# Kernel optimization log

Hardware: AMD Instinct MI355X
Metric: run time of the kernel (lower is better)

Reference implementation:

```python
import jax, jax.numpy as jnp
import numpy as np

H = 128  # hidden_size

def setup_inputs() -> dict:
    key = jax.random.key(0)
    ks = jax.random.split(key, 12)
    B, SEQ = 256, 1000
    static = jax.random.normal(ks[0], (B, 2, SEQ), jnp.float32)
    dynamic = jax.random.uniform(ks[1], (B, 2, SEQ), jnp.float32)
    # Encoder = 1x1 Conv1d(in_ch -> H): weight (H, in_ch), bias (H,)
    def xavier(k, shape):
        fan_in, fan_out = shape[1], shape[0]
        lim = np.sqrt(6.0 / (fan_in + fan_out)).astype(np.float32)
        return jax.random.uniform(k, shape, jnp.float32, -lim, lim)
    enc_s_w = xavier(ks[2], (H, 2)); enc_s_b = jnp.zeros((H,), jnp.float32)
    enc_d_w = xavier(ks[3], (H, 2)); enc_d_b = jnp.zeros((H,), jnp.float32)
    v = xavier(ks[4], (1, H))[0]                 # attention vector (H,)
    W = xavier(ks[5], (H, 3 * H))                # attention matrix (H, 3H)
    dense_w = xavier(ks[6], (H, 128)); dense_b = jnp.zeros((H,), jnp.float32)
    lin_w = xavier(ks[7], (1, H)); lin_b = jnp.zeros((1,), jnp.float32)
    return {"static": static, "dynamic": dynamic,
            "enc_s_w": enc_s_w, "enc_s_b": enc_s_b,
            "enc_d_w": enc_d_w, "enc_d_b": enc_d_b,
            "v": v, "W": W,
            "dense_w": dense_w, "dense_b": dense_b,
            "lin_w": lin_w, "lin_b": lin_b}


def reference(static, dynamic, enc_s_w, enc_s_b, enc_d_w, enc_d_b,
              v, W, dense_w, dense_b, lin_w, lin_b):
    B = static.shape[0]
    # 1x1-conv encoders (computed once; identical across loop iterations)
    e = jnp.einsum('hc,bcs->bhs', enc_s_w, static) + enc_s_b[None, :, None]   # (B,H,S)
    dyn_ld = jnp.broadcast_to(dynamic[:, 1:2, :], dynamic.shape)              # load channel expanded
    d = jnp.einsum('hc,bcs->bhs', enc_d_w, dyn_ld) + enc_d_b[None, :, None]   # (B,H,S)
    hy = jnp.zeros((B, H), static.dtype)
    for _ in range(3):  # fixed 3-step refinement loop
        hidden = jnp.concatenate(
            [e, d, jnp.broadcast_to(hy[:, :, None], e.shape)], axis=1)        # (B,3H,S)
        u = jnp.tanh(jnp.einsum('hk,bks->bhs', W, hidden))                    # (B,H,S)
        logit = jnp.einsum('h,bhs->bs', v, u)                                 # (B,S)
        prob = jax.nn.softmax(logit, axis=-1)
        hy = jnp.einsum('bs,bhs->bh', prob, e)                                # context update
    out = jax.nn.relu(hy @ dense_w.T + dense_b) @ lin_w.T + lin_b             # (B,1)
    return out
```

## Files before the change

kernel.cpp:

```cpp
#include <hip/hip_runtime.h>
#include <math.h>

#define HH  128
#define SS  1000
#define NT  1024
#define NW  (NT / 64)
#define C1 2.8853900817779268f
#define C2 1.4426950408889634f

typedef float v2f __attribute__((ext_vector_type(2)));

template <int CTRL>
__device__ __forceinline__ float dpp_add(float x) {
    int s = __builtin_amdgcn_update_dpp(0, __builtin_bit_cast(int, x),
                                        CTRL, 0xF, 0xF, true);
    return x + __builtin_bit_cast(float, s);
}


__global__ __launch_bounds__(NT) void sc_fold(
    const float* __restrict__ enc_s_w, const float* __restrict__ enc_s_b,
    const float* __restrict__ enc_d_w, const float* __restrict__ enc_d_b,
    const float* __restrict__ v, const float* __restrict__ W,
    float* __restrict__ ws) {
    const int t  = threadIdx.x;
    const int fh = blockIdx.x * 32 + (t >> 5);
    const int fq = t & 31;
    const float4* W1 = (const float4*)(W + fh * (3 * HH));
    const float4* W2 = (const float4*)(W + fh * (3 * HH) + HH);
    const float4* W3 = (const float4*)(W + fh * (3 * HH) + 2 * HH);
    const float4* ES = (const float4*)enc_s_w;
    const float4* ED = (const float4*)enc_d_w;
    const float4* SB = (const float4*)enc_s_b;
    const float4* DB = (const float4*)enc_d_b;
    const int k4 = fq;
    float4 w1 = W1[k4], w2 = W2[k4], w3 = W3[k4];
    float4 e01 = ES[2 * k4], e23 = ES[2 * k4 + 1];
    float4 d01 = ED[2 * k4], d23 = ED[2 * k4 + 1];
    float4 sb = SB[k4], db = DB[k4];
    float a0 = 0.f, a1 = 0.f, ad = 0.f, cc = 0.f, w30 = 0.f, w31 = 0.f, w3b = 0.f;
    a0 = fmaf(w1.x, e01.x, a0); a0 = fmaf(w1.y, e01.z, a0);
    a0 = fmaf(w1.z, e23.x, a0); a0 = fmaf(w1.w, e23.z, a0);
    a1 = fmaf(w1.x, e01.y, a1); a1 = fmaf(w1.y, e01.w, a1);
    a1 = fmaf(w1.z, e23.y, a1); a1 = fmaf(w1.w, e23.w, a1);
    ad = fmaf(w2.x, d01.x + d01.y, ad); ad = fmaf(w2.y, d01.z + d01.w, ad);
    ad = fmaf(w2.z, d23.x + d23.y, ad); ad = fmaf(w2.w, d23.z + d23.w, ad);
    cc = fmaf(w1.x, sb.x, cc); cc = fmaf(w1.y, sb.y, cc);
    cc = fmaf(w1.z, sb.z, cc); cc = fmaf(w1.w, sb.w, cc);
    cc = fmaf(w2.x, db.x, cc); cc = fmaf(w2.y, db.y, cc);
    cc = fmaf(w2.z, db.z, cc); cc = fmaf(w2.w, db.w, cc);
    w30 = fmaf(w3.x, e01.x, w30); w30 = fmaf(w3.y, e01.z, w30);
    w30 = fmaf(w3.z, e23.x, w30); w30 = fmaf(w3.w, e23.z, w30);
    w31 = fmaf(w3.x, e01.y, w31); w31 = fmaf(w3.y, e01.w, w31);
    w31 = fmaf(w3.z, e23.y, w31); w31 = fmaf(w3.w, e23.w, w31);
    w3b = fmaf(w3.x, sb.x, w3b); w3b = fmaf(w3.y, sb.y, w3b);
    w3b = fmaf(w3.z, sb.z, w3b); w3b = fmaf(w3.w, sb.w, w3b);
    a0  = dpp_add<0x111>(a0);  a0  = dpp_add<0x112>(a0);  a0  = dpp_add<0x114>(a0);
    a0  = dpp_add<0x118>(a0);  a0  = dpp_add<0x142>(a0);
    a1  = dpp_add<0x111>(a1);  a1  = dpp_add<0x112>(a1);  a1  = dpp_add<0x114>(a1);
    a1  = dpp_add<0x118>(a1);  a1  = dpp_add<0x142>(a1);
    ad  = dpp_add<0x111>(ad);  ad  = dpp_add<0x112>(ad);  ad  = dpp_add<0x114>(ad);
    ad  = dpp_add<0x118>(ad);  ad  = dpp_add<0x142>(ad);
    cc  = dpp_add<0x111>(cc);  cc  = dpp_add<0x112>(cc);  cc  = dpp_add<0x114>(cc);
    cc  = dpp_add<0x118>(cc);  cc  = dpp_add<0x142>(cc);
    w30 = dpp_add<0x111>(w30); w30 = dpp_add<0x112>(w30); w30 = dpp_add<0x114>(w30);
    w30 = dpp_add<0x118>(w30); w30 = dpp_add<0x142>(w30);
    w31 = dpp_add<0x111>(w31); w31 = dpp_add<0x112>(w31); w31 = dpp_add<0x114>(w31);
    w31 = dpp_add<0x118>(w31); w31 = dpp_add<0x142>(w31);
    w3b = dpp_add<0x111>(w3b); w3b = dpp_add<0x112>(w3b); w3b = dpp_add<0x114>(w3b);
    w3b = dpp_add<0x118>(w3b); w3b = dpp_add<0x142>(w3b);
    if (fq == 31) {
        ws[0 * HH + fh] = a0 * C1;
        ws[1 * HH + fh] = a1 * C1;
        ws[2 * HH + fh] = ad * C1;
        ws[4 * HH + fh] = cc * C1;
        ws[5 * HH + fh] = (cc + w3b) * C1;
        ws[6 * HH + fh] = w30 * C1;
        ws[7 * HH + fh] = w31 * C1;
    }
    if (blockIdx.x == 0) {
        if (t < HH) ws[3 * HH + t] = v[t];
        if (t < 32) {
            float4 x = ((const float4*)v)[t];
            float s = (x.x + x.y) + (x.z + x.w);
            #pragma unroll
            for (int off = 1; off < 32; off <<= 1) s += __shfl_xor(s, off);
            if (t == 0) ws[8 * HH] = s * C2;
        }
    }
}

#define OCTET(X, ACC)                                                         \
    {                                                                         \
        v2f vx0 = {X.x, X.x}, vx1 = {X.y, X.y}, vyv = {X.z, X.z};             \
        v2f z0 = __builtin_elementwise_fma(a0_0, vx0,                         \
                 __builtin_elementwise_fma(a1_0, vx1,                         \
                 __builtin_elementwise_fma(ad_0, vyv, cg_0)));                \
        v2f z1 = __builtin_elementwise_fma(a0_1, vx0,                         \
                 __builtin_elementwise_fma(a1_1, vx1,                         \
                 __builtin_elementwise_fma(ad_1, vyv, cg_1)));                \
        v2f z2 = __builtin_elementwise_fma(a0_2, vx0,                         \
                 __builtin_elementwise_fma(a1_2, vx1,                         \
                 __builtin_elementwise_fma(ad_2, vyv, cg_2)));                \
        v2f z3 = __builtin_elementwise_fma(a0_3, vx0,                         \
                 __builtin_elementwise_fma(a1_3, vx1,                         \
                 __builtin_elementwise_fma(ad_3, vyv, cg_3)));                \
        z0 = __builtin_elementwise_min(z0, clampv);                           \
        z1 = __builtin_elementwise_min(z1, clampv);                           \
        z2 = __builtin_elementwise_min(z2, clampv);                           \
        z3 = __builtin_elementwise_min(z3, clampv);                           \
        float e0 = __builtin_amdgcn_exp2f(z0.x);                              \
        float e1 = __builtin_amdgcn_exp2f(z0.y);                              \
        float e2 = __builtin_amdgcn_exp2f(z1.x);                              \
        float e3 = __builtin_amdgcn_exp2f(z1.y);                              \
        float e4 = __builtin_amdgcn_exp2f(z2.x);                              \
        float e5 = __builtin_amdgcn_exp2f(z2.y);                              \
        float e6 = __builtin_amdgcn_exp2f(z3.x);                              \
        float e7 = __builtin_amdgcn_exp2f(z3.y);                              \
        float tb0 = 1.f + e1, tb1 = 1.f + e3, tb2 = 1.f + e5, tb3 = 1.f + e7; \
        float d0 = fmaf(e0, tb0, tb0);                                        \
        float d1 = fmaf(e2, tb1, tb1);                                        \
        float d2 = fmaf(e4, tb2, tb2);                                        \
        float d3 = fmaf(e6, tb3, tb3);                                        \
        float n0 = fmaf(vv_0.x, e1, fmaf(vv_0.y, e0, cp0));                   \
        float n1 = fmaf(vv_1.x, e3, fmaf(vv_1.y, e2, cp1));                   \
        float n2 = fmaf(vv_2.x, e5, fmaf(vv_2.y, e4, cp2));                   \
        float n3 = fmaf(vv_3.x, e7, fmaf(vv_3.y, e6, cp3));                   \
        float Nq0 = fmaf(n0, d1, n1 * d0), Dq0 = d0 * d1;                     \
        float Nq1 = fmaf(n2, d3, n3 * d2), Dq1 = d2 * d3;                     \
        float Noc = fmaf(Nq0, Dq1, Nq1 * Dq0);                                \
        ACC = Noc * __builtin_amdgcn_rcpf(Dq0 * Dq1);                         \
        ACC = dpp_add<0x111>(ACC);                                            \
        ACC = dpp_add<0x112>(ACC);                                            \
        ACC = dpp_add<0x114>(ACC);                                            \
        ACC = dpp_add<0x118>(ACC);                                            \
    }

__global__ __launch_bounds__(NT, 4) void sc_main(
    const float* __restrict__ stat, const float* __restrict__ dyn,
    const float* __restrict__ ws,
    const float* __restrict__ enc_s_w, const float* __restrict__ enc_s_b,
    const float* __restrict__ dense_w, const float* __restrict__ dense_b,
    const float* __restrict__ lin_w, const float* __restrict__ lin_b,
    float* __restrict__ out) {
    const int b    = blockIdx.x;
    const int t    = threadIdx.x;
    const int wave = t >> 6;
    const int lane = t & 63;
    const int gl   = t & 15;
    const int sg   = t >> 4;

    __shared__ __align__(16) float4 xs[NT];
    __shared__ float4 red4[2][NW];
    __shared__ float hy_sh[HH];

    {
        float x0 = 0.f, x1 = 0.f, yv = 0.f;
        if (t < SS) {
            const float* sbp = stat + (size_t)b * 2 * SS;
            x0 = sbp[t];
            x1 = sbp[SS + t];
            yv = dyn[(size_t)b * 2 * SS + SS + t];
        }
        xs[t] = make_float4(x0, x1, yv, 0.f);
    }

    const int h0 = gl * 8;
    float4 u, u2;
    u = *(const float4*)(ws + 0 * HH + h0); u2 = *(const float4*)(ws + 0 * HH + h0 + 4);
    const v2f a0_0 = {u.x, u.y},  a0_1 = {u.z, u.w},
              a0_2 = {u2.x, u2.y}, a0_3 = {u2.z, u2.w};
    u = *(const float4*)(ws + 1 * HH + h0); u2 = *(const float4*)(ws + 1 * HH + h0 + 4);
    const v2f a1_0 = {u.x, u.y},  a1_1 = {u.z, u.w},
              a1_2 = {u2.x, u2.y}, a1_3 = {u2.z, u2.w};
    u = *(const float4*)(ws + 2 * HH + h0); u2 = *(const float4*)(ws + 2 * HH + h0 + 4);
    const v2f ad_0 = {u.x, u.y},  ad_1 = {u.z, u.w},
              ad_2 = {u2.x, u2.y}, ad_3 = {u2.z, u2.w};
    u = *(const float4*)(ws + 3 * HH + h0); u2 = *(const float4*)(ws + 3 * HH + h0 + 4);
    const v2f vv_0 = {u.x, u.y},  vv_1 = {u.z, u.w},
              vv_2 = {u2.x, u2.y}, vv_3 = {u2.z, u2.w};
    const float cp0 = vv_0.x + vv_0.y, cp1 = vv_1.x + vv_1.y;
    const float cp2 = vv_2.x + vv_2.y, cp3 = vv_3.x + vv_3.y;
    const float svc2 = ws[8 * HH];
    const v2f clampv = {14.f, 14.f};
    const bool ownerBase = (gl == 15);

    __syncthreads();

    float X0 = 0.f, X1 = 0.f;

    for (int iter = 0; iter < 3; ++iter) {
        v2f cg_0, cg_1, cg_2, cg_3;
        if (iter == 0) {
            u = *(const float4*)(ws + 4 * HH + h0);
            u2 = *(const float4*)(ws + 4 * HH + h0 + 4);
            cg_0 = (v2f){u.x, u.y};  cg_1 = (v2f){u.z, u.w};
            cg_2 = (v2f){u2.x, u2.y}; cg_3 = (v2f){u2.z, u2.w};
        } else {
            float4 b1 = *(const float4*)(ws + 5 * HH + h0);
            float4 b2 = *(const float4*)(ws + 5 * HH + h0 + 4);
            float4 p1 = *(const float4*)(ws + 6 * HH + h0);
            float4 p2 = *(const float4*)(ws + 6 * HH + h0 + 4);
            float4 q1 = *(const float4*)(ws + 7 * HH + h0);
            float4 q2 = *(const float4*)(ws + 7 * HH + h0 + 4);
            v2f X0v = {X0, X0}, X1v = {X1, X1};
            cg_0 = __builtin_elementwise_fma(
                (v2f){p1.x, p1.y}, X0v,
                __builtin_elementwise_fma((v2f){q1.x, q1.y}, X1v, (v2f){b1.x, b1.y}));
            cg_1 = __builtin_elementwise_fma(
                (v2f){p1.z, p1.w}, X0v,
                __builtin_elementwise_fma((v2f){q1.z, q1.w}, X1v, (v2f){b1.z, b1.w}));
            cg_2 = __builtin_elementwise_fma(
                (v2f){p2.x, p2.y}, X0v,
                __builtin_elementwise_fma((v2f){q2.x, q2.y}, X1v, (v2f){b2.x, b2.y}));
            cg_3 = __builtin_elementwise_fma(
                (v2f){p2.z, p2.w}, X0v,
                __builtin_elementwise_fma((v2f){q2.z, q2.w}, X1v, (v2f){b2.z, b2.w}));
        }

        float S = 0.f, Sx0 = 0.f, Sx1 = 0.f;
        #pragma unroll 2
        for (int pass = 0; pass < 8; ++pass) {
            const int sA = pass * 64 + sg;
            const int sB = 512 + sA;
            float4 xA = xs[sA];
            float4 xB = xs[sB];
            float accA, accB;
            OCTET(xA, accA);
            OCTET(xB, accB);
            float argA = ownerBase ? fmaf(-C1, accA, svc2) : -200.f;
            const bool ownB = ownerBase && (sB < SS);
            float argB = ownB ? fmaf(-C1, accB, svc2) : -200.f;
            float pA = __builtin_amdgcn_exp2f(argA);
            float pB = __builtin_amdgcn_exp2f(argB);
            S   += pA + pB;
            Sx0  = fmaf(pA, xA.x, fmaf(pB, xB.x, Sx0));
            Sx1  = fmaf(pA, xA.y, fmaf(pB, xB.y, Sx1));
        }
        S   += __shfl_xor(S, 16);   S   += __shfl_xor(S, 32);
        Sx0 += __shfl_xor(Sx0, 16); Sx0 += __shfl_xor(Sx0, 32);
        Sx1 += __shfl_xor(Sx1, 16); Sx1 += __shfl_xor(Sx1, 32);
        if (lane == 15) red4[iter & 1][wave] = make_float4(S, Sx0, Sx1, 0.f);
        __syncthreads();
        float4 w4 = red4[iter & 1][lane & 15];
        #pragma unroll
        for (int off = 1; off < 16; off <<= 1) {
            w4.x += __shfl_xor(w4.x, off);
            w4.y += __shfl_xor(w4.y, off);
            w4.z += __shfl_xor(w4.z, off);
        }
        float inv = __builtin_amdgcn_rcpf(w4.x);
        X0 = w4.y * inv;
        X1 = w4.z * inv;
    }

    if (t < HH)
        hy_sh[t] = fmaf(enc_s_w[2 * t], X0, fmaf(enc_s_w[2 * t + 1], X1, enc_s_b[t]));
    __syncthreads();

    float o = 0.f;
    if (t < HH) {
        const float4* dw4 = (const float4*)(dense_w + t * HH);
        const float4* hy4 = (const float4*)hy_sh;
        float r = dense_b[t];
        #pragma unroll 4
        for (int k = 0; k < HH / 4; ++k) {
            float4 d4 = dw4[k], h4v = hy4[k];
            r = fmaf(d4.x, h4v.x, fmaf(d4.y, h4v.y, fmaf(d4.z, h4v.z, fmaf(d4.w, h4v.w, r))));
        }
        o = lin_w[t] * fmaxf(r, 0.f);
    }
    #pragma unroll
    for (int off = 32; off > 0; off >>= 1) o += __shfl_xor(o, off);
    if (lane == 0) red4[0][wave].x = o;
    __syncthreads();
    if (t == 0) {
        float s = 0.f;
        for (int i = 0; i < NW; ++i) s += red4[0][i].x;
        out[b] = s + lin_b[0];
    }
}

extern "C" void kernel_launch(void* const* d_in, const int* in_sizes, int n_in,
                              void* d_out, int out_size, void* d_ws, size_t ws_size,
                              hipStream_t stream) {
    const float* stat    = (const float*)d_in[0];
    const float* dyn     = (const float*)d_in[1];
    const float* enc_s_w = (const float*)d_in[2];
    const float* enc_s_b = (const float*)d_in[3];
    const float* enc_d_w = (const float*)d_in[4];
    const float* enc_d_b = (const float*)d_in[5];
    const float* v       = (const float*)d_in[6];
    const float* W       = (const float*)d_in[7];
    const float* dense_w = (const float*)d_in[8];
    const float* dense_b = (const float*)d_in[9];
    const float* lin_w   = (const float*)d_in[10];
    const float* lin_b   = (const float*)d_in[11];
    float* out = (float*)d_out;
    float* ws  = (float*)d_ws;

    const int B = in_sizes[0] / (2 * SS);

    hipLaunchKernelGGL(sc_fold, dim3(4), dim3(NT), 0, stream,
                       enc_s_w, enc_s_b, enc_d_w, enc_d_b, v, W, ws);
    hipLaunchKernelGGL(sc_main, dim3(B), dim3(NT), 0, stream,
                       stat, dyn, ws, enc_s_w, enc_s_b, dense_w, dense_b,
                       lin_w, lin_b, out);
}
```

Measured before the change: 40.71 us.

## Fuse weight-folding prologue into main kernel, dropping separate fold launch

Removes the small sc_fold kernel and has every block of the main kernel recompute the folded attention coefficients into shared memory before the refinement loop. This drops one kernel launch and the dependency gap between the two launches, and replaces global workspace reads with LDS reads. In exchange each of the 256 blocks redundantly reads W (about 196 KB, mostly served from cache) and does the fold arithmetic, and adds 4 KB of shared memory per block.

```diff
diff --git a/kernel.cpp b/kernel.cpp
--- a/kernel.cpp
+++ b/kernel.cpp
@@ -15,79 +15,6 @@
     int s = __builtin_amdgcn_update_dpp(0, __builtin_bit_cast(int, x),
                                         CTRL, 0xF, 0xF, true);
     return x + __builtin_bit_cast(float, s);
-}
-
-
-__global__ __launch_bounds__(NT) void sc_fold(
-    const float* __restrict__ enc_s_w, const float* __restrict__ enc_s_b,
-    const float* __restrict__ enc_d_w, const float* __restrict__ enc_d_b,
-    const float* __restrict__ v, const float* __restrict__ W,
-    float* __restrict__ ws) {
-    const int t  = threadIdx.x;
-    const int fh = blockIdx.x * 32 + (t >> 5);
-    const int fq = t & 31;
-    const float4* W1 = (const float4*)(W + fh * (3 * HH));
-    const float4* W2 = (const float4*)(W + fh * (3 * HH) + HH);
-    const float4* W3 = (const float4*)(W + fh * (3 * HH) + 2 * HH);
-    const float4* ES = (const float4*)enc_s_w;
-    const float4* ED = (const float4*)enc_d_w;
-    const float4* SB = (const float4*)enc_s_b;
-    const float4* DB = (const float4*)enc_d_b;
-    const int k4 = fq;
-    float4 w1 = W1[k4], w2 = W2[k4], w3 = W3[k4];
-    float4 e01 = ES[2 * k4], e23 = ES[2 * k4 + 1];
-    float4 d01 = ED[2 * k4], d23 = ED[2 * k4 + 1];
-    float4 sb = SB[k4], db = DB[k4];
-    float a0 = 0.f, a1 = 0.f, ad = 0.f, cc = 0.f, w30 = 0.f, w31 = 0.f, w3b = 0.f;
-    a0 = fmaf(w1.x, e01.x, a0); a0 = fmaf(w1.y, e01.z, a0);
-    a0 = fmaf(w1.z, e23.x, a0); a0 = fmaf(w1.w, e23.z, a0);
-    a1 = fmaf(w1.x, e01.y, a1); a1 = fmaf(w1.y, e01.w, a1);
-    a1 = fmaf(w1.z, e23.y, a1); a1 = fmaf(w1.w, e23.w, a1);
-    ad = fmaf(w2.x, d01.x + d01.y, ad); ad = fmaf(w2.y, d01.z + d01.w, ad);
-    ad = fmaf(w2.z, d23.x + d23.y, ad); ad = fmaf(w2.w, d23.z + d23.w, ad);
-    cc = fmaf(w1.x, sb.x, cc); cc = fmaf(w1.y, sb.y, cc);
-    cc = fmaf(w1.z, sb.z, cc); cc = fmaf(w1.w, sb.w, cc);
-    cc = fmaf(w2.x, db.x, cc); cc = fmaf(w2.y, db.y, cc);
-    cc = fmaf(w2.z, db.z, cc); cc = fmaf(w2.w, db.w, cc);
-    w30 = fmaf(w3.x, e01.x, w30); w30 = fmaf(w3.y, e01.z, w30);
-    w30 = fmaf(w3.z, e23.x, w30); w30 = fmaf(w3.w, e23.z, w30);
-    w31 = fmaf(w3.x, e01.y, w31); w31 = fmaf(w3.y, e01.w, w31);
-    w31 = fmaf(w3.z, e23.y, w31); w31 = fmaf(w3.w, e23.w, w31);
-    w3b = fmaf(w3.x, sb.x, w3b); w3b = fmaf(w3.y, sb.y, w3b);
-    w3b = fmaf(w3.z, sb.z, w3b); w3b = fmaf(w3.w, sb.w, w3b);
-    a0  = dpp_add<0x111>(a0);  a0  = dpp_add<0x112>(a0);  a0  = dpp_add<0x114>(a0);
-    a0  = dpp_add<0x118>(a0);  a0  = dpp_add<0x142>(a0);
-    a1  = dpp_add<0x111>(a1);  a1  = dpp_add<0x112>(a1);  a1  = dpp_add<0x114>(a1);
-    a1  = dpp_add<0x118>(a1);  a1  = dpp_add<0x142>(a1);
-    ad  = dpp_add<0x111>(ad);  ad  = dpp_add<0x112>(ad);  ad  = dpp_add<0x114>(ad);
-    ad  = dpp_add<0x118>(ad);  ad  = dpp_add<0x142>(ad);
-    cc  = dpp_add<0x111>(cc);  cc  = dpp_add<0x112>(cc);  cc  = dpp_add<0x114>(cc);
-    cc  = dpp_add<0x118>(cc);  cc  = dpp_add<0x142>(cc);
-    w30 = dpp_add<0x111>(w30); w30 = dpp_add<0x112>(w30); w30 = dpp_add<0x114>(w30);
-    w30 = dpp_add<0x118>(w30); w30 = dpp_add<0x142>(w30);
-    w31 = dpp_add<0x111>(w31); w31 = dpp_add<0x112>(w31); w31 = dpp_add<0x114>(w31);
-    w31 = dpp_add<0x118>(w31); w31 = dpp_add<0x142>(w31);
-    w3b = dpp_add<0x111>(w3b); w3b = dpp_add<0x112>(w3b); w3b = dpp_add<0x114>(w3b);
-    w3b = dpp_add<0x118>(w3b); w3b = dpp_add<0x142>(w3b);
-    if (fq == 31) {
-        ws[0 * HH + fh] = a0 * C1;
-        ws[1 * HH + fh] = a1 * C1;
-        ws[2 * HH + fh] = ad * C1;
-        ws[4 * HH + fh] = cc * C1;
-        ws[5 * HH + fh] = (cc + w3b) * C1;
-        ws[6 * HH + fh] = w30 * C1;
-        ws[7 * HH + fh] = w31 * C1;
-    }
-    if (blockIdx.x == 0) {
-        if (t < HH) ws[3 * HH + t] = v[t];
-        if (t < 32) {
-            float4 x = ((const float4*)v)[t];
-            float s = (x.x + x.y) + (x.z + x.w);
-            #pragma unroll
-            for (int off = 1; off < 32; off <<= 1) s += __shfl_xor(s, off);
-            if (t == 0) ws[8 * HH] = s * C2;
-        }
-    }
 }
 
 #define OCTET(X, ACC)                                                         \
@@ -136,10 +63,11 @@
         ACC = dpp_add<0x118>(ACC);                                            \
     }
 
-__global__ __launch_bounds__(NT, 4) void sc_main(
+__global__ __launch_bounds__(NT, 4) void sc_all(
     const float* __restrict__ stat, const float* __restrict__ dyn,
-    const float* __restrict__ ws,
     const float* __restrict__ enc_s_w, const float* __restrict__ enc_s_b,
+    const float* __restrict__ enc_d_w, const float* __restrict__ enc_d_b,
+    const float* __restrict__ v, const float* __restrict__ W,
     const float* __restrict__ dense_w, const float* __restrict__ dense_b,
     const float* __restrict__ lin_w, const float* __restrict__ lin_b,
     float* __restrict__ out) {
@@ -151,8 +79,10 @@
     const int sg   = t >> 4;
 
     __shared__ __align__(16) float4 xs[NT];
+    __shared__ __align__(16) float kc[8][HH];
     __shared__ float4 red4[2][NW];
     __shared__ float hy_sh[HH];
+    __shared__ float svc2_sh;
 
     {
         float x0 = 0.f, x1 = 0.f, yv = 0.f;
@@ -165,44 +95,104 @@
         xs[t] = make_float4(x0, x1, yv, 0.f);
     }
 
+    {
+        const int fh = t >> 3;
+        const int fq = t & 7;
+        const float4* W1 = (const float4*)(W + fh * (3 * HH));
+        const float4* W2 = (const float4*)(W + fh * (3 * HH) + HH);
+        const float4* W3 = (const float4*)(W + fh * (3 * HH) + 2 * HH);
+        const float4* ES = (const float4*)enc_s_w;
+        const float4* ED = (const float4*)enc_d_w;
+        const float4* SB = (const float4*)enc_s_b;
+        const float4* DB = (const float4*)enc_d_b;
+        float a0 = 0.f, a1 = 0.f, ad = 0.f, cc = 0.f, w30 = 0.f, w31 = 0.f, w3b = 0.f;
+        #pragma unroll
+        for (int j = 0; j < 4; ++j) {
+            const int k4 = fq * 4 + j;
+            float4 w1 = W1[k4], w2 = W2[k4], w3 = W3[k4];
+            float4 e01 = ES[2 * k4], e23 = ES[2 * k4 + 1];
+            float4 d01 = ED[2 * k4], d23 = ED[2 * k4 + 1];
+            float4 sb = SB[k4], db = DB[k4];
+            a0 = fmaf(w1.x, e01.x, a0); a0 = fmaf(w1.y, e01.z, a0);
+            a0 = fmaf(w1.z, e23.x, a0); a0 = fmaf(w1.w, e23.z, a0);
+            a1 = fmaf(w1.x, e01.y, a1); a1 = fmaf(w1.y, e01.w, a1);
+            a1 = fmaf(w1.z, e23.y, a1); a1 = fmaf(w1.w, e23.w, a1);
+            ad = fmaf(w2.x, d01.x + d01.y, ad); ad = fmaf(w2.y, d01.z + d01.w, ad);
+            ad = fmaf(w2.z, d23.x + d23.y, ad); ad = fmaf(w2.w, d23.z + d23.w, ad);
+            cc = fmaf(w1.x, sb.x, cc); cc = fmaf(w1.y, sb.y, cc);
+            cc = fmaf(w1.z, sb.z, cc); cc = fmaf(w1.w, sb.w, cc);
+            cc = fmaf(w2.x, db.x, cc); cc = fmaf(w2.y, db.y, cc);
+            cc = fmaf(w2.z, db.z, cc); cc = fmaf(w2.w, db.w, cc);
+            w30 = fmaf(w3.x, e01.x, w30); w30 = fmaf(w3.y, e01.z, w30);
+            w30 = fmaf(w3.z, e23.x, w30); w30 = fmaf(w3.w, e23.z, w30);
+            w31 = fmaf(w3.x, e01.y, w31); w31 = fmaf(w3.y, e01.w, w31);
+            w31 = fmaf(w3.z, e23.y, w31); w31 = fmaf(w3.w, e23.w, w31);
+            w3b = fmaf(w3.x, sb.x, w3b); w3b = fmaf(w3.y, sb.y, w3b);
+            w3b = fmaf(w3.z, sb.z, w3b); w3b = fmaf(w3.w, sb.w, w3b);
+        }
+        a0  = dpp_add<0x111>(a0);  a0  = dpp_add<0x112>(a0);  a0  = dpp_add<0x114>(a0);
+        a1  = dpp_add<0x111>(a1);  a1  = dpp_add<0x112>(a1);  a1  = dpp_add<0x114>(a1);
+        ad  = dpp_add<0x111>(ad);  ad  = dpp_add<0x112>(ad);  ad  = dpp_add<0x114>(ad);
+        cc  = dpp_add<0x111>(cc);  cc  = dpp_add<0x112>(cc);  cc  = dpp_add<0x114>(cc);
+        w30 = dpp_add<0x111>(w30); w30 = dpp_add<0x112>(w30); w30 = dpp_add<0x114>(w30);
+        w31 = dpp_add<0x111>(w31); w31 = dpp_add<0x112>(w31); w31 = dpp_add<0x114>(w31);
+        w3b = dpp_add<0x111>(w3b); w3b = dpp_add<0x112>(w3b); w3b = dpp_add<0x114>(w3b);
+        if (fq == 7) {
+            kc[0][fh] = a0 * C1;
+            kc[1][fh] = a1 * C1;
+            kc[2][fh] = ad * C1;
+            kc[4][fh] = cc * C1;
+            kc[5][fh] = (cc + w3b) * C1;
+            kc[6][fh] = w30 * C1;
+            kc[7][fh] = w31 * C1;
+        }
+        if (t < HH) kc[3][t] = v[t];
+        if (t < 32) {
+            float4 x = ((const float4*)v)[t];
+            float s = (x.x + x.y) + (x.z + x.w);
+            #pragma unroll
+            for (int off = 1; off < 32; off <<= 1) s += __shfl_xor(s, off);
+            if (t == 0) svc2_sh = s * C2;
+        }
+    }
+    __syncthreads();
+
     const int h0 = gl * 8;
     float4 u, u2;
-    u = *(const float4*)(ws + 0 * HH + h0); u2 = *(const float4*)(ws + 0 * HH + h0 + 4);
+    u = *(const float4*)&kc[0][h0]; u2 = *(const float4*)&kc[0][h0 + 4];
     const v2f a0_0 = {u.x, u.y},  a0_1 = {u.z, u.w},
               a0_2 = {u2.x, u2.y}, a0_3 = {u2.z, u2.w};
-    u = *(const float4*)(ws + 1 * HH + h0); u2 = *(const float4*)(ws + 1 * HH + h0 + 4);
+    u = *(const float4*)&kc[1][h0]; u2 = *(const float4*)&kc[1][h0 + 4];
     const v2f a1_0 = {u.x, u.y},  a1_1 = {u.z, u.w},
               a1_2 = {u2.x, u2.y}, a1_3 = {u2.z, u2.w};
-    u = *(const float4*)(ws + 2 * HH + h0); u2 = *(const float4*)(ws + 2 * HH + h0 + 4);
+    u = *(const float4*)&kc[2][h0]; u2 = *(const float4*)&kc[2][h0 + 4];
     const v2f ad_0 = {u.x, u.y},  ad_1 = {u.z, u.w},
               ad_2 = {u2.x, u2.y}, ad_3 = {u2.z, u2.w};
-    u = *(const float4*)(ws + 3 * HH + h0); u2 = *(const float4*)(ws + 3 * HH + h0 + 4);
+    u = *(const float4*)&kc[3][h0]; u2 = *(const float4*)&kc[3][h0 + 4];
     const v2f vv_0 = {u.x, u.y},  vv_1 = {u.z, u.w},
               vv_2 = {u2.x, u2.y}, vv_3 = {u2.z, u2.w};
     const float cp0 = vv_0.x + vv_0.y, cp1 = vv_1.x + vv_1.y;
     const float cp2 = vv_2.x + vv_2.y, cp3 = vv_3.x + vv_3.y;
-    const float svc2 = ws[8 * HH];
+    const float svc2 = svc2_sh;
     const v2f clampv = {14.f, 14.f};
     const bool ownerBase = (gl == 15);
-
-    __syncthreads();
 
     float X0 = 0.f, X1 = 0.f;
 
     for (int iter = 0; iter < 3; ++iter) {
         v2f cg_0, cg_1, cg_2, cg_3;
         if (iter == 0) {
-            u = *(const float4*)(ws + 4 * HH + h0);
-            u2 = *(const float4*)(ws + 4 * HH + h0 + 4);
+            u = *(const float4*)&kc[4][h0];
+            u2 = *(const float4*)&kc[4][h0 + 4];
             cg_0 = (v2f){u.x, u.y};  cg_1 = (v2f){u.z, u.w};
             cg_2 = (v2f){u2.x, u2.y}; cg_3 = (v2f){u2.z, u2.w};
         } else {
-            float4 b1 = *(const float4*)(ws + 5 * HH + h0);
-            float4 b2 = *(const float4*)(ws + 5 * HH + h0 + 4);
-            float4 p1 = *(const float4*)(ws + 6 * HH + h0);
-            float4 p2 = *(const float4*)(ws + 6 * HH + h0 + 4);
-            float4 q1 = *(const float4*)(ws + 7 * HH + h0);
-            float4 q2 = *(const float4*)(ws + 7 * HH + h0 + 4);
+            float4 b1 = *(const float4*)&kc[5][h0];
+            float4 b2 = *(const float4*)&kc[5][h0 + 4];
+            float4 p1 = *(const float4*)&kc[6][h0];
+            float4 p2 = *(const float4*)&kc[6][h0 + 4];
+            float4 q1 = *(const float4*)&kc[7][h0];
+            float4 q2 = *(const float4*)&kc[7][h0 + 4];
             v2f X0v = {X0, X0}, X1v = {X1, X1};
             cg_0 = __builtin_elementwise_fma(
                 (v2f){p1.x, p1.y}, X0v,
@@ -297,13 +287,10 @@
     const float* lin_w   = (const float*)d_in[10];
     const float* lin_b   = (const float*)d_in[11];
     float* out = (float*)d_out;
-    float* ws  = (float*)d_ws;
 
     const int B = in_sizes[0] / (2 * SS);
 
-    hipLaunchKernelGGL(sc_fold, dim3(4), dim3(NT), 0, stream,
-                       enc_s_w, enc_s_b, enc_d_w, enc_d_b, v, W, ws);
-    hipLaunchKernelGGL(sc_main, dim3(B), dim3(NT), 0, stream,
-                       stat, dyn, ws, enc_s_w, enc_s_b, dense_w, dense_b,
-                       lin_w, lin_b, out);
+    hipLaunchKernelGGL(sc_all, dim3(B), dim3(NT), 0, stream,
+                       stat, dyn, enc_s_w, enc_s_b, enc_d_w, enc_d_b, v, W,
+                       dense_w, dense_b, lin_w, lin_b, out);
 }
```

New measurement: 46.91 us. 15.2% more time.
